# Kernel optimization log

Hardware: AMD Instinct MI355X
Metric: run time of the kernel (lower is better)

## Reference

```python
import jax, jax.numpy as jnp
import numpy as np

B, S, I, H, O, L = 256, 512, 256, 256, 256, 64


def setup_inputs() -> dict:
    key = jax.random.key(0)
    ks = jax.random.split(key, 12)
    def lin(k, fan_in, fan_out):
        kw, kb = jax.random.split(k)
        lim = 1.0 / np.sqrt(fan_in)
        W = jax.random.uniform(kw, (fan_in, fan_out), jnp.float32, -lim, lim)
        b = jax.random.uniform(kb, (fan_out,), jnp.float32, -lim, lim)
        return W, b
    x = jax.random.normal(ks[0], (B, S, I), jnp.float32)
    W1x, b1x = lin(ks[1], I, H)   # rnn1.Wax
    W1a, b1a = lin(ks[2], H, H)   # rnn1.Waa
    W2x, b2x = lin(ks[3], O, H)   # rnn2.Wax
    W2a, b2a = lin(ks[4], H, H)   # rnn2.Waa
    Wy, by = lin(ks[5], H, O)     # Wya
    return {"x": x, "W1x": W1x, "b1x": b1x, "W1a": W1a, "b1a": b1a,
            "W2x": W2x, "b2x": b2x, "W2a": W2a, "b2a": b2a, "Wy": Wy, "by": by}


def reference(x, W1x, b1x, W1a, b1a, W2x, b2x, W2a, b2a, Wy, by):
    batch = x.shape[0]
    a0 = jnp.zeros((batch, W1a.shape[0]), x.dtype)  # a[:, -1] is zeros at encoder start

    # Encoder: a_t = tanh(Wax(x_t) + Waa(a_{t-1}))
    def enc_step(a, x_t):
        a = jnp.tanh(x_t @ W1x + b1x + a @ W1a + b1a)
        return a, None
    a_last, _ = jax.lax.scan(enc_step, a0, jnp.swapaxes(x, 0, 1))  # [S,B,I] scan

    # Torch code: y_pred[:,0] set from encoder, then decoder reads y_pred[:,i]
    # BEFORE overwriting it -> input is y0 at i=0, zeros for i>0.
    y0 = jax.nn.sigmoid(a_last @ Wy + by)  # [B,O]
    zero_in = jnp.zeros_like(y0)

    def dec_step(a, i):
        inp = jnp.where(i == 0, y0, zero_in)
        a = jnp.tanh(inp @ W2x + b2x + a @ W2a + b2a)
        y = jax.nn.sigmoid(a @ Wy + by)
        return a, y
    _, ys = jax.lax.scan(dec_step, a_last, jnp.arange(L))  # ys: [L,B,O]
    return jnp.swapaxes(ys, 0, 1)  # [B,L,O]
```

## Files before the change

### kernel.cpp

```cpp
#include <hip/hip_runtime.h>

typedef unsigned short u16;
typedef unsigned int   u32;
typedef __attribute__((ext_vector_type(8))) __bf16 bf16x8;
typedef __attribute__((ext_vector_type(8))) u16    u16x8;
typedef __attribute__((ext_vector_type(4))) float  f32x4;
typedef __attribute__((ext_vector_type(4))) u32    u32x4;
typedef __attribute__((ext_vector_type(2))) u32    u32x2;

#define MFMA16(a,b,c) __builtin_amdgcn_mfma_f32_16x16x32_bf16((a),(b),(c),0,0,0)
#define C_TANH 2.8853900817779268f
#define NL2E  -1.4426950408889634f

__device__ __forceinline__ float ubit(u32 x){ return __builtin_bit_cast(float, x); }
__device__ __forceinline__ u16 f2b(float f){
    u32 b = __builtin_bit_cast(u32, f);
    b += 0x7FFFu + ((b >> 16) & 1u);
    return (u16)(b >> 16);
}
__device__ __forceinline__ u32 pkbf(float a, float b){ return ((u32)f2b(b) << 16) | (u32)f2b(a); }
__device__ __forceinline__ u32 pk_away(float a, float b){
    u32 ua = (__builtin_bit_cast(u32, a) + 0x8000u) >> 16;
    u32 ub = (__builtin_bit_cast(u32, b) + 0x8000u) & 0xFFFF0000u;
    return ub | ua;
}
__device__ __forceinline__ void bar_lds(){ __asm__ volatile("s_waitcnt lgkmcnt(0)\n\ts_barrier" ::: "memory"); }

__global__ __launch_bounds__(256, 1) void k1_xw(const float* __restrict__ x, const float* __restrict__ w1x,
                                               const float* __restrict__ b1x, const float* __restrict__ b1a,
                                               u16* __restrict__ xpre)
{
    const int t = blockIdx.x;
    const int tid = threadIdx.x, lane = tid & 63, w = tid >> 6;
    const int l15 = lane & 15, q = lane >> 4;
    const int cw = w * 64;

    bf16x8 bw[4][8];
    f32x4 biasv[4];
    #pragma unroll
    for (int nt = 0; nt < 4; ++nt){
        const int n0 = cw + nt * 16 + q * 4;
        f32x4 bx = *(const f32x4*)(b1x + n0);
        f32x4 ba = *(const f32x4*)(b1a + n0);
        biasv[nt] = (bx + ba) * C_TANH;
        const int n = cw + nt * 16 + l15;
        #pragma unroll
        for (int ks = 0; ks < 8; ++ks){
            u16x8 tt;
            #pragma unroll
            for (int j = 0; j < 8; ++j) tt[j] = f2b(w1x[(ks * 32 + q * 8 + j) * 256 + n] * C_TANH);
            bw[nt][ks] = __builtin_bit_cast(bf16x8, tt);
        }
    }

    for (int blk = 0; blk < 16; ++blk){
        const int b0r = blk * 16;
        bf16x8 av[8];
        #pragma unroll
        for (int ks = 0; ks < 8; ++ks){
            const float* p = x + ((size_t)(b0r + l15) * 512 + t) * 256 + ks * 32 + q * 8;
            f32x4 v0 = *(const f32x4*)p;
            f32x4 v1 = *(const f32x4*)(p + 4);
            u32x4 dd = { pkbf(v0[0], v0[1]), pkbf(v0[2], v0[3]),
                         pkbf(v1[0], v1[1]), pkbf(v1[2], v1[3]) };
            av[ks] = __builtin_bit_cast(bf16x8, dd);
        }
        f32x4 acc[4];
        #pragma unroll
        for (int nt = 0; nt < 4; ++nt) acc[nt] = biasv[nt];
        #pragma unroll
        for (int ks = 0; ks < 8; ++ks)
            #pragma unroll
            for (int nt = 0; nt < 4; ++nt)
                acc[nt] = MFMA16(bw[nt][ks], av[ks], acc[nt]);
        const int bg = blk * 4 + (l15 >> 2), b4 = l15 & 3;
        #pragma unroll
        for (int p2 = 0; p2 < 2; ++p2){
            const size_t a16 = ((((size_t)t * 64 + bg) * 8 + (w * 2 + p2)) * 16 + q * 4 + b4) * 8;
            u32x4 V = { pkbf(acc[p2 * 2][0], acc[p2 * 2][1]), pkbf(acc[p2 * 2][2], acc[p2 * 2][3]),
                        pkbf(acc[p2 * 2 + 1][0], acc[p2 * 2 + 1][1]), pkbf(acc[p2 * 2 + 1][2], acc[p2 * 2 + 1][3]) };
            *(u32x4*)(xpre + a16) = V;
        }
    }
}

__global__ __launch_bounds__(512, 2) void k2_enc(const float* __restrict__ w1a, const u16* __restrict__ xpre,
                                                u16* __restrict__ alast)
{
    __shared__ __align__(16) u16 st[2][4][272];
    const int tid = threadIdx.x, lane = tid & 63, w = tid >> 6;
    const int l15 = lane & 15, q = lane >> 4;
    const int b4 = l15 & 3;
    const bool selnt = (l15 & 4) != 0, selrp = (l15 & 8) != 0;
    const int wcol = w * 32 + (selnt ? 16 : 0) + q * 4 + (selrp ? 2 : 0);
    const int bg = blockIdx.x;

    bf16x8 bw[2][8];
    #pragma unroll
    for (int nt = 0; nt < 2; ++nt){
        const int n = w * 32 + nt * 16 + l15;
        #pragma unroll
        for (int ks = 0; ks < 8; ++ks){
            u16x8 tt;
            #pragma unroll
            for (int j = 0; j < 8; ++j) tt[j] = f2b(w1a[(ks * 32 + q * 8 + j) * 256 + n] * C_TANH);
            bw[nt][ks] = __builtin_bit_cast(bf16x8, tt);
        }
    }
    for (int i = tid; i < 4 * 272; i += 512) (&st[0][0][0])[i] = 0;
    __syncthreads();

    const u16* xp = xpre + (((size_t)bg * 8 + w) * 16 + q * 4 + b4) * 8;
    u32x4 c = *(const u32x4*)xp;
    u32x4 a = *(const u32x4*)(xp + 65536);

    const u16 (*sR)[272] = st[0];
    u16 (*sW)[272] = st[1];

    for (int t = 0; t < 512; ++t){
        const size_t tp = (size_t)((t + 2 < 512) ? t + 2 : 511) * 65536;
        u32x4 n_ = *(const u32x4*)(xp + tp);

        bf16x8 av[8];
        #pragma unroll
        for (int ks = 0; ks < 8; ++ks)
            av[ks] = *(const bf16x8*)&sR[b4][ks * 32 + q * 8];

        f32x4 acc[2];
        #pragma unroll
        for (int nt = 0; nt < 2; ++nt)
            #pragma unroll
            for (int r = 0; r < 4; ++r){
                const u32 d = c[nt * 2 + (r >> 1)];
                acc[nt][r] = ubit((r & 1) ? (d & 0xFFFF0000u) : (d << 16));
            }
        #pragma unroll
        for (int ks = 0; ks < 8; ++ks)
            #pragma unroll
            for (int nt = 0; nt < 2; ++nt)
                acc[nt] = MFMA16(bw[nt][ks], av[ks], acc[nt]);

        const float s0 = selnt ? acc[1][0] : acc[0][0];
        const float s1 = selnt ? acc[1][1] : acc[0][1];
        const float s2 = selnt ? acc[1][2] : acc[0][2];
        const float s3 = selnt ? acc[1][3] : acc[0][3];
        const float mv0 = selrp ? s2 : s0;
        const float mv1 = selrp ? s3 : s1;
        const float e0 = __builtin_amdgcn_exp2f(mv0);
        const float t0 = 1.0f - 2.0f * __builtin_amdgcn_rcpf(e0 + 1.0f);
        const float e1 = __builtin_amdgcn_exp2f(mv1);
        const float t1 = 1.0f - 2.0f * __builtin_amdgcn_rcpf(e1 + 1.0f);
        *(u32*)&sW[b4][wcol] = pk_away(t0, t1);

        c = a; a = n_;
        bar_lds();
        const u16 (*tmp)[272] = sR; sR = (const u16(*)[272])sW; sW = (u16(*)[272])tmp;
    }
    if (tid < 128){
        const int row = tid >> 5, c8 = (tid & 31) * 8;
        *(u32x4*)(alast + (size_t)(bg * 4 + row) * 256 + c8) = *(const u32x4*)&sR[row][c8];
    }
}

__global__ __launch_bounds__(256, 1) void k3_pre(const float* __restrict__ wy, const float* __restrict__ by,
                                                const float* __restrict__ w2x,
                                                const u16* __restrict__ alast, float* __restrict__ injws)
{
    __shared__ __align__(16) u16 st[16][264];
    __shared__ __align__(16) u16 y0s[16][264];
    const int tid = threadIdx.x, lane = tid & 63, w = tid >> 6;
    const int l15 = lane & 15, q = lane >> 4;
    const int bg = blockIdx.x;
    {
        const int row = tid >> 4, c = (tid & 15) * 16;
        #pragma unroll
        for (int j = 0; j < 2; ++j)
            *(u32x4*)&st[row][c + j * 8] = *(const u32x4*)(alast + (size_t)(bg * 16 + row) * 256 + c + j * 8);
    }
    __syncthreads();
    {
        bf16x8 bwy[4][8];
        f32x4 biasy[4];
        #pragma unroll
        for (int nt = 0; nt < 4; ++nt){
            const int n0 = w * 64 + nt * 16 + q * 4;
            biasy[nt] = (*(const f32x4*)(by + n0)) * NL2E;
            const int n = w * 64 + nt * 16 + l15;
            #pragma unroll
            for (int ks = 0; ks < 8; ++ks){
                u16x8 tt;
                #pragma unroll
                for (int j = 0; j < 8; ++j) tt[j] = f2b(wy[(ks * 32 + q * 8 + j) * 256 + n] * NL2E);
                bwy[nt][ks] = __builtin_bit_cast(bf16x8, tt);
            }
        }
        bf16x8 av[8];
        #pragma unroll
        for (int ks = 0; ks < 8; ++ks) av[ks] = *(const bf16x8*)&st[l15][ks * 32 + q * 8];
        f32x4 acc[4];
        #pragma unroll
        for (int nt = 0; nt < 4; ++nt) acc[nt] = biasy[nt];
        #pragma unroll
        for (int ks = 0; ks < 8; ++ks)
            #pragma unroll
            for (int nt = 0; nt < 4; ++nt) acc[nt] = MFMA16(bwy[nt][ks], av[ks], acc[nt]);
        #pragma unroll
        for (int nt = 0; nt < 4; ++nt){
            float y[4];
            #pragma unroll
            for (int r = 0; r < 4; ++r) y[r] = __builtin_amdgcn_rcpf(1.0f + __builtin_amdgcn_exp2f(acc[nt][r]));
            u32x2 hp = { pkbf(y[0], y[1]), pkbf(y[2], y[3]) };
            *(u32x2*)&y0s[l15][w * 64 + nt * 16 + q * 4] = hp;
        }
    }
    __syncthreads();
    {
        bf16x8 av[8];
        #pragma unroll
        for (int ks = 0; ks < 8; ++ks) av[ks] = *(const bf16x8*)&y0s[l15][ks * 32 + q * 8];
        f32x4 acc[4];
        #pragma unroll
        for (int nt = 0; nt < 4; ++nt) acc[nt] = (f32x4){0.f, 0.f, 0.f, 0.f};
        #pragma unroll
        for (int ks = 0; ks < 8; ++ks)
            #pragma unroll
            for (int nt = 0; nt < 4; ++nt){
                const int n = w * 64 + nt * 16 + l15;
                u16x8 tt;
                #pragma unroll
                for (int j = 0; j < 8; ++j) tt[j] = f2b(w2x[(ks * 32 + q * 8 + j) * 256 + n] * C_TANH);
                acc[nt] = MFMA16(__builtin_bit_cast(bf16x8, tt), av[ks], acc[nt]);
            }
        const int bgr = bg * 4 + (l15 >> 2), b4 = l15 & 3;
        #pragma unroll
        for (int p2 = 0; p2 < 2; ++p2){
            const size_t ib = (((size_t)bgr * 8 + (size_t)(w * 2 + p2)) * 16 + q * 4 + b4) * 8;
            *(f32x4*)(injws + ib)     = acc[p2 * 2];
            *(f32x4*)(injws + ib + 4) = acc[p2 * 2 + 1];
        }
    }
}

__global__ __launch_bounds__(512, 2) void k3_rec(const float* __restrict__ w2a, const float* __restrict__ b2x,
                                                const float* __restrict__ b2a, const u16* __restrict__ alast,
                                                const float* __restrict__ injws, u16* __restrict__ astate)
{
    __shared__ __align__(16) u16 st[2][4][272];
    const int tid = threadIdx.x, lane = tid & 63, w = tid >> 6;
    const int l15 = lane & 15, q = lane >> 4;
    const int b4 = l15 & 3;
    const bool selnt = (l15 & 4) != 0, selrp = (l15 & 8) != 0;
    const int wcol = w * 32 + (selnt ? 16 : 0) + q * 4 + (selrp ? 2 : 0);
    const int bg = blockIdx.x;

    bf16x8 bw[2][8];
    f32x4 bias2[2];
    #pragma unroll
    for (int nt = 0; nt < 2; ++nt){
        const int n0 = w * 32 + nt * 16 + q * 4;
        f32x4 bx = *(const f32x4*)(b2x + n0);
        f32x4 ba = *(const f32x4*)(b2a + n0);
        bias2[nt] = (bx + ba) * C_TANH;
        const int n = w * 32 + nt * 16 + l15;
        #pragma unroll
        for (int ks = 0; ks < 8; ++ks){
            u16x8 tt;
            #pragma unroll
            for (int j = 0; j < 8; ++j) tt[j] = f2b(w2a[(ks * 32 + q * 8 + j) * 256 + n] * C_TANH);
            bw[nt][ks] = __builtin_bit_cast(bf16x8, tt);
        }
    }
    f32x4 ini[2];
    {
        const size_t ib = (((size_t)bg * 8 + w) * 16 + q * 4 + b4) * 8;
        #pragma unroll
        for (int nt = 0; nt < 2; ++nt)
            ini[nt] = *(const f32x4*)(injws + ib + nt * 4) + bias2[nt];
    }
    if (tid < 128){
        const int row = tid >> 5, c8 = (tid & 31) * 8;
        *(u32x4*)&st[0][row][c8] = *(const u32x4*)(alast + (size_t)(bg * 4 + row) * 256 + c8);
    }
    __syncthreads();

    const u16 (*sR)[272] = st[0];
    u16 (*sW)[272] = st[1];

    for (int i = 0; i < 64; ++i){
        bf16x8 av[8];
        #pragma unroll
        for (int ks = 0; ks < 8; ++ks) av[ks] = *(const bf16x8*)&sR[b4][ks * 32 + q * 8];
        f32x4 acc[2];
        #pragma unroll
        for (int nt = 0; nt < 2; ++nt) acc[nt] = ini[nt];
        #pragma unroll
        for (int ks = 0; ks < 8; ++ks)
            #pragma unroll
            for (int nt = 0; nt < 2; ++nt) acc[nt] = MFMA16(bw[nt][ks], av[ks], acc[nt]);

        const float s0 = selnt ? acc[1][0] : acc[0][0];
        const float s1 = selnt ? acc[1][1] : acc[0][1];
        const float s2 = selnt ? acc[1][2] : acc[0][2];
        const float s3 = selnt ? acc[1][3] : acc[0][3];
        const float mv0 = selrp ? s2 : s0;
        const float mv1 = selrp ? s3 : s1;
        const float e0 = __builtin_amdgcn_exp2f(mv0);
        const float t0 = 1.0f - 2.0f * __builtin_amdgcn_rcpf(e0 + 1.0f);
        const float e1 = __builtin_amdgcn_exp2f(mv1);
        const float t1 = 1.0f - 2.0f * __builtin_amdgcn_rcpf(e1 + 1.0f);
        const u32 hp = pk_away(t0, t1);
        *(u32*)&sW[b4][wcol] = hp;
        *(u32*)(astate + ((size_t)i * 256 + bg * 4 + b4) * 256 + wcol) = hp;

        if (i == 0){
            #pragma unroll
            for (int nt = 0; nt < 2; ++nt) ini[nt] = bias2[nt];
        }
        bar_lds();
        const u16 (*tmp)[272] = sR; sR = (const u16(*)[272])sW; sW = (u16(*)[272])tmp;
    }
}

__global__ __launch_bounds__(256, 1) void k3_out(const float* __restrict__ wy, const float* __restrict__ by,
                                                const u16* __restrict__ astate, float* __restrict__ out)
{
    const int tid = threadIdx.x, lane = tid & 63, w = tid >> 6;
    const int l15 = lane & 15, q = lane >> 4;

    bf16x8 bwy[4][8];
    f32x4 biasy[4];
    #pragma unroll
    for (int nt = 0; nt < 4; ++nt){
        const int n0 = w * 64 + nt * 16 + q * 4;
        biasy[nt] = (*(const f32x4*)(by + n0)) * NL2E;
        const int n = w * 64 + nt * 16 + l15;
        #pragma unroll
        for (int ks = 0; ks < 8; ++ks){
            u16x8 tt;
            #pragma unroll
            for (int j = 0; j < 8; ++j) tt[j] = f2b(wy[(ks * 32 + q * 8 + j) * 256 + n] * NL2E);
            bwy[nt][ks] = __builtin_bit_cast(bf16x8, tt);
        }
    }
    #pragma unroll
    for (int tix = 0; tix < 4; ++tix){
        const int R0 = (blockIdx.x * 4 + tix) * 16;
        bf16x8 av[8];
        #pragma unroll
        for (int ks = 0; ks < 8; ++ks)
            av[ks] = *(const bf16x8*)(astate + (size_t)(R0 + l15) * 256 + ks * 32 + q * 8);
        f32x4 acc[4];
        #pragma unroll
        for (int nt = 0; nt < 4; ++nt) acc[nt] = biasy[nt];
        #pragma unroll
        for (int ks = 0; ks < 8; ++ks)
            #pragma unroll
            for (int nt = 0; nt < 4; ++nt) acc[nt] = MFMA16(bwy[nt][ks], av[ks], acc[nt]);
        const int R = R0 + l15, ii = R >> 8, b = R & 255;
        #pragma unroll
        for (int nt = 0; nt < 4; ++nt){
            f32x4 o4;
            #pragma unroll
            for (int r = 0; r < 4; ++r)
                o4[r] = __builtin_amdgcn_rcpf(1.0f + __builtin_amdgcn_exp2f(acc[nt][r]));
            *(f32x4*)(out + ((size_t)b * 64 + ii) * 256 + w * 64 + nt * 16 + q * 4) = o4;
        }
    }
}

extern "C" void kernel_launch(void* const* d_in, const int* in_sizes, int n_in,
                              void* d_out, int out_size, void* d_ws, size_t ws_size,
                              hipStream_t stream) {
    const float* x   = (const float*)d_in[0];
    const float* w1x = (const float*)d_in[1];
    const float* b1x = (const float*)d_in[2];
    const float* w1a = (const float*)d_in[3];
    const float* b1a = (const float*)d_in[4];
    const float* w2x = (const float*)d_in[5];
    const float* b2x = (const float*)d_in[6];
    const float* w2a = (const float*)d_in[7];
    const float* b2a = (const float*)d_in[8];
    const float* wy  = (const float*)d_in[9];
    const float* by  = (const float*)d_in[10];

    u16*   xpre   = (u16*)d_ws;
    u16*   astate = (u16*)d_ws;
    u16*   alast  = xpre + (size_t)512 * 16 * 512 * 8;
    float* injws  = (float*)(alast + 256 * 256);
    float* o      = (float*)d_out;

    k1_xw <<<512, 256, 0, stream>>>(x, w1x, b1x, b1a, xpre);
    k2_enc<<<64,  512, 0, stream>>>(w1a, xpre, alast);
    k3_pre<<<16,  256, 0, stream>>>(wy, by, w2x, alast, injws);
    k3_rec<<<64,  512, 0, stream>>>(w2a, b2x, b2a, alast, injws, astate);
    k3_out<<<256, 256, 0, stream>>>(wy, by, astate, o);
}
```

Measured before the change: 555.1 us.

## Fuse encoder, decoder-init and decoder recurrence into one kernel

Merges the encoder recurrence, the y0/input-injection precompute and the decoder recurrence into a single k2_full kernel. Each block computes y0 and the W2x injection for its own four batch rows in registers and LDS, so the alast and injws round-trips and two kernel launches disappear. The decoder state layout in the workspace changes, and k3_out is updated to match. It also raises wave priority around the MFMA chains, and the decoder state now overwrites the start of the xpre region while other blocks may still be running the encoder. That relies on all blocks progressing in rough lockstep.

```diff
diff --git a/kernel.cpp b/kernel.cpp
--- a/kernel.cpp
+++ b/kernel.cpp
@@ -84,8 +84,10 @@
     }
 }
 
-__global__ __launch_bounds__(512, 2) void k2_enc(const float* __restrict__ w1a, const u16* __restrict__ xpre,
-                                                u16* __restrict__ alast)
+__global__ __launch_bounds__(512, 2) void k2_full(const float* __restrict__ w1a, const float* __restrict__ wy,
+                                                 const float* __restrict__ by,  const float* __restrict__ w2x,
+                                                 const float* __restrict__ w2a, const float* __restrict__ b2x,
+                                                 const float* __restrict__ b2a, u16* ws)
 {
     __shared__ __align__(16) u16 st[2][4][272];
     const int tid = threadIdx.x, lane = tid & 63, w = tid >> 6;
@@ -110,7 +112,7 @@
     for (int i = tid; i < 4 * 272; i += 512) (&st[0][0][0])[i] = 0;
     __syncthreads();
 
-    const u16* xp = xpre + (((size_t)bg * 8 + w) * 16 + q * 4 + b4) * 8;
+    const u16* xp = ws + (((size_t)bg * 8 + w) * 16 + q * 4 + b4) * 8;
     u32x4 c = *(const u32x4*)xp;
     u32x4 a = *(const u32x4*)(xp + 65536);
 
@@ -134,11 +136,13 @@
                 const u32 d = c[nt * 2 + (r >> 1)];
                 acc[nt][r] = ubit((r & 1) ? (d & 0xFFFF0000u) : (d << 16));
             }
+        __builtin_amdgcn_s_setprio(1);
         #pragma unroll
         for (int ks = 0; ks < 8; ++ks)
             #pragma unroll
             for (int nt = 0; nt < 2; ++nt)
                 acc[nt] = MFMA16(bw[nt][ks], av[ks], acc[nt]);
+        __builtin_amdgcn_s_setprio(0);
 
         const float s0 = selnt ? acc[1][0] : acc[0][0];
         const float s1 = selnt ? acc[1][1] : acc[0][1];
@@ -156,36 +160,15 @@
         bar_lds();
         const u16 (*tmp)[272] = sR; sR = (const u16(*)[272])sW; sW = (u16(*)[272])tmp;
     }
-    if (tid < 128){
-        const int row = tid >> 5, c8 = (tid & 31) * 8;
-        *(u32x4*)(alast + (size_t)(bg * 4 + row) * 256 + c8) = *(const u32x4*)&sR[row][c8];
-    }
-}
-
-__global__ __launch_bounds__(256, 1) void k3_pre(const float* __restrict__ wy, const float* __restrict__ by,
-                                                const float* __restrict__ w2x,
-                                                const u16* __restrict__ alast, float* __restrict__ injws)
-{
-    __shared__ __align__(16) u16 st[16][264];
-    __shared__ __align__(16) u16 y0s[16][264];
-    const int tid = threadIdx.x, lane = tid & 63, w = tid >> 6;
-    const int l15 = lane & 15, q = lane >> 4;
-    const int bg = blockIdx.x;
+
     {
-        const int row = tid >> 4, c = (tid & 15) * 16;
-        #pragma unroll
-        for (int j = 0; j < 2; ++j)
-            *(u32x4*)&st[row][c + j * 8] = *(const u32x4*)(alast + (size_t)(bg * 16 + row) * 256 + c + j * 8);
-    }
-    __syncthreads();
-    {
-        bf16x8 bwy[4][8];
-        f32x4 biasy[4];
-        #pragma unroll
-        for (int nt = 0; nt < 4; ++nt){
-            const int n0 = w * 64 + nt * 16 + q * 4;
+        bf16x8 bwy[2][8];
+        f32x4 biasy[2];
+        #pragma unroll
+        for (int nt = 0; nt < 2; ++nt){
+            const int n0 = w * 32 + nt * 16 + q * 4;
             biasy[nt] = (*(const f32x4*)(by + n0)) * NL2E;
-            const int n = w * 64 + nt * 16 + l15;
+            const int n = w * 32 + nt * 16 + l15;
             #pragma unroll
             for (int ks = 0; ks < 8; ++ks){
                 u16x8 tt;
@@ -196,95 +179,65 @@
         }
         bf16x8 av[8];
         #pragma unroll
-        for (int ks = 0; ks < 8; ++ks) av[ks] = *(const bf16x8*)&st[l15][ks * 32 + q * 8];
-        f32x4 acc[4];
-        #pragma unroll
-        for (int nt = 0; nt < 4; ++nt) acc[nt] = biasy[nt];
-        #pragma unroll
-        for (int ks = 0; ks < 8; ++ks)
-            #pragma unroll
-            for (int nt = 0; nt < 4; ++nt) acc[nt] = MFMA16(bwy[nt][ks], av[ks], acc[nt]);
-        #pragma unroll
-        for (int nt = 0; nt < 4; ++nt){
-            float y[4];
-            #pragma unroll
-            for (int r = 0; r < 4; ++r) y[r] = __builtin_amdgcn_rcpf(1.0f + __builtin_amdgcn_exp2f(acc[nt][r]));
-            u32x2 hp = { pkbf(y[0], y[1]), pkbf(y[2], y[3]) };
-            *(u32x2*)&y0s[l15][w * 64 + nt * 16 + q * 4] = hp;
-        }
-    }
-    __syncthreads();
+        for (int ks = 0; ks < 8; ++ks) av[ks] = *(const bf16x8*)&sR[b4][ks * 32 + q * 8];
+        f32x4 acc[2];
+        #pragma unroll
+        for (int nt = 0; nt < 2; ++nt) acc[nt] = biasy[nt];
+        #pragma unroll
+        for (int ks = 0; ks < 8; ++ks)
+            #pragma unroll
+            for (int nt = 0; nt < 2; ++nt) acc[nt] = MFMA16(bwy[nt][ks], av[ks], acc[nt]);
+        const float s0 = selnt ? acc[1][0] : acc[0][0];
+        const float s1 = selnt ? acc[1][1] : acc[0][1];
+        const float s2 = selnt ? acc[1][2] : acc[0][2];
+        const float s3 = selnt ? acc[1][3] : acc[0][3];
+        const float mv0 = selrp ? s2 : s0;
+        const float mv1 = selrp ? s3 : s1;
+        const float y0v = __builtin_amdgcn_rcpf(1.0f + __builtin_amdgcn_exp2f(mv0));
+        const float y1v = __builtin_amdgcn_rcpf(1.0f + __builtin_amdgcn_exp2f(mv1));
+        *(u32*)&sW[b4][wcol] = pkbf(y0v, y1v);
+    }
+    bar_lds();
+
+    f32x4 ini[2];
+    f32x4 bias2[2];
     {
-        bf16x8 av[8];
-        #pragma unroll
-        for (int ks = 0; ks < 8; ++ks) av[ks] = *(const bf16x8*)&y0s[l15][ks * 32 + q * 8];
-        f32x4 acc[4];
-        #pragma unroll
-        for (int nt = 0; nt < 4; ++nt) acc[nt] = (f32x4){0.f, 0.f, 0.f, 0.f};
-        #pragma unroll
-        for (int ks = 0; ks < 8; ++ks)
-            #pragma unroll
-            for (int nt = 0; nt < 4; ++nt){
-                const int n = w * 64 + nt * 16 + l15;
+        bf16x8 av2[8];
+        #pragma unroll
+        for (int ks = 0; ks < 8; ++ks) av2[ks] = *(const bf16x8*)&sW[b4][ks * 32 + q * 8];
+        bar_lds();
+        #pragma unroll
+        for (int nt = 0; nt < 2; ++nt){
+            const int n0 = w * 32 + nt * 16 + q * 4;
+            f32x4 bx = *(const f32x4*)(b2x + n0);
+            f32x4 ba = *(const f32x4*)(b2a + n0);
+            bias2[nt] = (bx + ba) * C_TANH;
+            ini[nt] = (f32x4){0.f, 0.f, 0.f, 0.f};
+        }
+        #pragma unroll
+        for (int ks = 0; ks < 8; ++ks)
+            #pragma unroll
+            for (int nt = 0; nt < 2; ++nt){
+                const int n = w * 32 + nt * 16 + l15;
                 u16x8 tt;
                 #pragma unroll
                 for (int j = 0; j < 8; ++j) tt[j] = f2b(w2x[(ks * 32 + q * 8 + j) * 256 + n] * C_TANH);
-                acc[nt] = MFMA16(__builtin_bit_cast(bf16x8, tt), av[ks], acc[nt]);
+                ini[nt] = MFMA16(__builtin_bit_cast(bf16x8, tt), av2[ks], ini[nt]);
             }
-        const int bgr = bg * 4 + (l15 >> 2), b4 = l15 & 3;
-        #pragma unroll
-        for (int p2 = 0; p2 < 2; ++p2){
-            const size_t ib = (((size_t)bgr * 8 + (size_t)(w * 2 + p2)) * 16 + q * 4 + b4) * 8;
-            *(f32x4*)(injws + ib)     = acc[p2 * 2];
-            *(f32x4*)(injws + ib + 4) = acc[p2 * 2 + 1];
-        }
-    }
-}
-
-__global__ __launch_bounds__(512, 2) void k3_rec(const float* __restrict__ w2a, const float* __restrict__ b2x,
-                                                const float* __restrict__ b2a, const u16* __restrict__ alast,
-                                                const float* __restrict__ injws, u16* __restrict__ astate)
-{
-    __shared__ __align__(16) u16 st[2][4][272];
-    const int tid = threadIdx.x, lane = tid & 63, w = tid >> 6;
-    const int l15 = lane & 15, q = lane >> 4;
-    const int b4 = l15 & 3;
-    const bool selnt = (l15 & 4) != 0, selrp = (l15 & 8) != 0;
-    const int wcol = w * 32 + (selnt ? 16 : 0) + q * 4 + (selrp ? 2 : 0);
-    const int bg = blockIdx.x;
-
-    bf16x8 bw[2][8];
-    f32x4 bias2[2];
-    #pragma unroll
-    for (int nt = 0; nt < 2; ++nt){
-        const int n0 = w * 32 + nt * 16 + q * 4;
-        f32x4 bx = *(const f32x4*)(b2x + n0);
-        f32x4 ba = *(const f32x4*)(b2a + n0);
-        bias2[nt] = (bx + ba) * C_TANH;
-        const int n = w * 32 + nt * 16 + l15;
-        #pragma unroll
-        for (int ks = 0; ks < 8; ++ks){
-            u16x8 tt;
-            #pragma unroll
-            for (int j = 0; j < 8; ++j) tt[j] = f2b(w2a[(ks * 32 + q * 8 + j) * 256 + n] * C_TANH);
-            bw[nt][ks] = __builtin_bit_cast(bf16x8, tt);
-        }
-    }
-    f32x4 ini[2];
-    {
-        const size_t ib = (((size_t)bg * 8 + w) * 16 + q * 4 + b4) * 8;
-        #pragma unroll
-        for (int nt = 0; nt < 2; ++nt)
-            ini[nt] = *(const f32x4*)(injws + ib + nt * 4) + bias2[nt];
-    }
-    if (tid < 128){
-        const int row = tid >> 5, c8 = (tid & 31) * 8;
-        *(u32x4*)&st[0][row][c8] = *(const u32x4*)(alast + (size_t)(bg * 4 + row) * 256 + c8);
-    }
-    __syncthreads();
-
-    const u16 (*sR)[272] = st[0];
-    u16 (*sW)[272] = st[1];
+        #pragma unroll
+        for (int nt = 0; nt < 2; ++nt) ini[nt] = ini[nt] + bias2[nt];
+        #pragma unroll
+        for (int nt = 0; nt < 2; ++nt){
+            const int n = w * 32 + nt * 16 + l15;
+            #pragma unroll
+            for (int ks = 0; ks < 8; ++ks){
+                u16x8 tt;
+                #pragma unroll
+                for (int j = 0; j < 8; ++j) tt[j] = f2b(w2a[(ks * 32 + q * 8 + j) * 256 + n] * C_TANH);
+                bw[nt][ks] = __builtin_bit_cast(bf16x8, tt);
+            }
+        }
+    }
 
     for (int i = 0; i < 64; ++i){
         bf16x8 av[8];
@@ -293,10 +246,12 @@
         f32x4 acc[2];
         #pragma unroll
         for (int nt = 0; nt < 2; ++nt) acc[nt] = ini[nt];
+        __builtin_amdgcn_s_setprio(1);
         #pragma unroll
         for (int ks = 0; ks < 8; ++ks)
             #pragma unroll
             for (int nt = 0; nt < 2; ++nt) acc[nt] = MFMA16(bw[nt][ks], av[ks], acc[nt]);
+        __builtin_amdgcn_s_setprio(0);
 
         const float s0 = selnt ? acc[1][0] : acc[0][0];
         const float s1 = selnt ? acc[1][1] : acc[0][1];
@@ -310,7 +265,7 @@
         const float t1 = 1.0f - 2.0f * __builtin_amdgcn_rcpf(e1 + 1.0f);
         const u32 hp = pk_away(t0, t1);
         *(u32*)&sW[b4][wcol] = hp;
-        *(u32*)(astate + ((size_t)i * 256 + bg * 4 + b4) * 256 + wcol) = hp;
+        *(u32*)(ws + (((size_t)(i * 64 + bg)) << 10) + b4 * 256 + wcol) = hp;
 
         if (i == 0){
             #pragma unroll
@@ -345,10 +300,12 @@
     #pragma unroll
     for (int tix = 0; tix < 4; ++tix){
         const int R0 = (blockIdx.x * 4 + tix) * 16;
-        bf16x8 av[8];
-        #pragma unroll
-        for (int ks = 0; ks < 8; ++ks)
-            av[ks] = *(const bf16x8*)(astate + (size_t)(R0 + l15) * 256 + ks * 32 + q * 8);
+        const int Rl = R0 + l15, iiL = Rl >> 8, bL = Rl & 255;
+        const u16* ap = astate + (((size_t)(iiL * 64 + (bL >> 2))) << 10) + (size_t)(bL & 3) * 256;
+        bf16x8 av[8];
+        #pragma unroll
+        for (int ks = 0; ks < 8; ++ks)
+            av[ks] = *(const bf16x8*)(ap + ks * 32 + q * 8);
         f32x4 acc[4];
         #pragma unroll
         for (int nt = 0; nt < 4; ++nt) acc[nt] = biasy[nt];
@@ -356,14 +313,13 @@
         for (int ks = 0; ks < 8; ++ks)
             #pragma unroll
             for (int nt = 0; nt < 4; ++nt) acc[nt] = MFMA16(bwy[nt][ks], av[ks], acc[nt]);
-        const int R = R0 + l15, ii = R >> 8, b = R & 255;
         #pragma unroll
         for (int nt = 0; nt < 4; ++nt){
             f32x4 o4;
             #pragma unroll
             for (int r = 0; r < 4; ++r)
                 o4[r] = __builtin_amdgcn_rcpf(1.0f + __builtin_amdgcn_exp2f(acc[nt][r]));
-            *(f32x4*)(out + ((size_t)b * 64 + ii) * 256 + w * 64 + nt * 16 + q * 4) = o4;
+            *(f32x4*)(out + ((size_t)bL * 64 + iiL) * 256 + w * 64 + nt * 16 + q * 4) = o4;
         }
     }
 }
@@ -383,15 +339,10 @@
     const float* wy  = (const float*)d_in[9];
     const float* by  = (const float*)d_in[10];
 
-    u16*   xpre   = (u16*)d_ws;
-    u16*   astate = (u16*)d_ws;
-    u16*   alast  = xpre + (size_t)512 * 16 * 512 * 8;
-    float* injws  = (float*)(alast + 256 * 256);
-    float* o      = (float*)d_out;
-
-    k1_xw <<<512, 256, 0, stream>>>(x, w1x, b1x, b1a, xpre);
-    k2_enc<<<64,  512, 0, stream>>>(w1a, xpre, alast);
-    k3_pre<<<16,  256, 0, stream>>>(wy, by, w2x, alast, injws);
-    k3_rec<<<64,  512, 0, stream>>>(w2a, b2x, b2a, alast, injws, astate);
-    k3_out<<<256, 256, 0, stream>>>(wy, by, astate, o);
-}
+    u16*   ws16 = (u16*)d_ws;
+    float* o    = (float*)d_out;
+
+    k1_xw  <<<512, 256, 0, stream>>>(x, w1x, b1x, b1a, ws16);
+    k2_full<<<64,  512, 0, stream>>>(w1a, wy, by, w2x, w2a, b2x, b2a, ws16);
+    k3_out <<<256, 256, 0, stream>>>(wy, by, ws16, o);
+}
```

Measured after the change: 534.0 us. 3.8% less time.
